# Performance work log

Measured on AMD Instinct MI355X. Metric: run time of the kernel, lower is better.

Reference implementation:

```python
import jax, jax.numpy as jnp
import numpy as np

NUM_LATENTS = 8192
LATENT_DIM = 256


def setup_inputs() -> dict:
    key = jax.random.key(0)
    kx, kw = jax.random.split(key)
    x = jax.random.normal(kx, (32, 512, LATENT_DIM), dtype=jnp.float32)
    # codebook init: uniform(-1/K, 1/K), matching nn.Embedding init in the module
    bound = 1.0 / NUM_LATENTS
    codebook = jax.random.uniform(
        kw, (NUM_LATENTS, LATENT_DIM), dtype=jnp.float32, minval=-bound, maxval=bound
    )
    return {"x": x, "codebook": codebook}


def reference(x, codebook):
    # torch.cdist(x, W) followed by argmin. Since sqrt is monotone, argmin over
    # squared Euclidean distance gives identical indices; we expand
    x2 = jnp.sum(x * x, axis=-1, keepdims=True)              # [B, T, 1]
    w2 = jnp.sum(codebook * codebook, axis=-1)               # [K]
    xw = jnp.einsum("btd,kd->btk", x, codebook)              # [B, T, K]
    dist2 = x2 - 2.0 * xw + w2                               # [B, T, K]
    indices = jnp.argmin(dist2, axis=-1)                     # [B, T] int
    z = codebook[indices]                                    # [B, T, D]
    # straight-through estimator: z_q = x + stop_grad(z - x)
    z_q = x + jax.lax.stop_gradient(z - x)
    return (z_q, z, x, indices)
```

## Files before the change

### kernel.cpp

```cpp
#include <hip/hip_runtime.h>
#include <hip/hip_bf16.h>
#include <cstddef>
#include <cstdint>

#define M_TOK   16384
#define N_CODE  8192
#define K_DIM   256
#define NSPLIT  4
#define BM      128
#define BN      128
#define BK      32

typedef short bf16x8 __attribute__((ext_vector_type(8)));
typedef float f32x4  __attribute__((ext_vector_type(4)));

__device__ __forceinline__ unsigned short f2bf_rne(float f) {
    unsigned u = __float_as_uint(f);
    unsigned r = u + 0x7FFFu + ((u >> 16) & 1u);
    return (unsigned short)(r >> 16);
}
__device__ __forceinline__ float bf2f(unsigned short h) {
    union { unsigned u; float f; } c; c.u = ((unsigned)h) << 16; return c.f;
}

__device__ __forceinline__ void gload16(const void* g, void* l) {
    __builtin_amdgcn_global_load_lds(
        (const __attribute__((address_space(1))) void*)g,
        (__attribute__((address_space(3))) void*)l, 16, 0, 0);
}

__global__ void vq_prep(const float* __restrict__ x, const float* __restrict__ cb,
                        unsigned short* __restrict__ xh, unsigned short* __restrict__ xl,
                        unsigned short* __restrict__ wh, unsigned short* __restrict__ wl,
                        float* __restrict__ x2, float* __restrict__ w2) {
    int gt   = blockIdx.x * blockDim.x + threadIdx.x;
    int row  = gt >> 6;
    int lane = gt & 63;
    if (row >= M_TOK + N_CODE) return;
    const float* src; unsigned short *dh, *dl; float* dn;
    if (row < M_TOK) {
        src = x + (size_t)row * K_DIM;
        dh = xh + (size_t)row * K_DIM; dl = xl + (size_t)row * K_DIM; dn = x2 + row;
    } else {
        int r = row - M_TOK;
        src = cb + (size_t)r * K_DIM;
        dh = wh + (size_t)r * K_DIM; dl = wl + (size_t)r * K_DIM; dn = w2 + r;
    }
    float4 v = ((const float4*)src)[lane];
    unsigned short h0 = f2bf_rne(v.x), h1 = f2bf_rne(v.y);
    unsigned short h2 = f2bf_rne(v.z), h3 = f2bf_rne(v.w);
    unsigned short l0 = f2bf_rne(v.x - bf2f(h0)), l1 = f2bf_rne(v.y - bf2f(h1));
    unsigned short l2 = f2bf_rne(v.z - bf2f(h2)), l3 = f2bf_rne(v.w - bf2f(h3));
    ushort4 hv; hv.x = h0; hv.y = h1; hv.z = h2; hv.w = h3;
    ushort4 lv; lv.x = l0; lv.y = l1; lv.z = l2; lv.w = l3;
    ((ushort4*)dh)[lane] = hv;
    ((ushort4*)dl)[lane] = lv;
    float s = v.x*v.x + v.y*v.y + v.z*v.z + v.w*v.w;
    #pragma unroll
    for (int off = 32; off > 0; off >>= 1) s += __shfl_down(s, off);
    if (lane == 0) *dn = s;
}

__global__ __launch_bounds__(256, 2)
void vq_main_mfma(const unsigned short* __restrict__ xh, const unsigned short* __restrict__ xl,
                  const unsigned short* __restrict__ wh, const unsigned short* __restrict__ wl,
                  const float* __restrict__ x2, const float* __restrict__ w2,
                  float* __restrict__ pminv, int* __restrict__ pmini) {
    __shared__ unsigned short xh_s[BM][BK];
    __shared__ unsigned short xl_s[BM][BK];
    __shared__ unsigned short wh_s[BN][BK];
    __shared__ unsigned short wl_s[BN][BK];
    __shared__ float red_d[BM][2];
    __shared__ int   red_i[BM][2];

    const int split = blockIdx.x;
    const int mtile = blockIdx.y;
    const int gm    = mtile * BM;
    const int tid   = threadIdx.x;
    const int w     = tid >> 6;
    const int lane  = tid & 63;
    const int wr    = w >> 1;
    const int wc    = w & 1;
    const int quad  = lane >> 4;
    const int l15   = lane & 15;

    const int w32   = w * 32;
    const int srow  = (lane >> 2);
    const int sc16  = (lane & 3) * 16;

    float x2r[16];
    #pragma unroll
    for (int rt = 0; rt < 4; ++rt)
        #pragma unroll
        for (int reg = 0; reg < 4; ++reg)
            x2r[rt*4+reg] = x2[gm + wr*64 + rt*16 + quad*4 + reg];

    float minv[16];
    int   mini[16];
    #pragma unroll
    for (int i = 0; i < 16; ++i) { minv[i] = 3.4e38f; mini[i] = 0; }

    const char* xhp = (const char*)xh;
    const char* xlp = (const char*)xl;
    const char* whp = (const char*)wh;
    const char* wlp = (const char*)wl;

    const int tiles = (N_CODE / NSPLIT) / BN;
    for (int tile = 0; tile < tiles; ++tile) {
        const int nb = split * (N_CODE / NSPLIT) + tile * BN;

        f32x4 acc[4][4];
        #pragma unroll
        for (int rt = 0; rt < 4; ++rt)
            #pragma unroll
            for (int ct = 0; ct < 4; ++ct)
                acc[rt][ct] = (f32x4){0.f, 0.f, 0.f, 0.f};

        for (int kc = 0; kc < K_DIM / BK; ++kc) {
            __syncthreads();
            #pragma unroll
            for (int i = 0; i < 2; ++i) {
                int r = w32 + i * 16 + srow;
                size_t xoff = (size_t)(gm + r) * (K_DIM*2) + kc*(BK*2) + sc16;
                size_t woff = (size_t)(nb + r) * (K_DIM*2) + kc*(BK*2) + sc16;
                unsigned ldso = (unsigned)(w32 + i * 16) * (BK*2);
                gload16(xhp + xoff, (char*)&xh_s[0][0] + ldso);
                gload16(xlp + xoff, (char*)&xl_s[0][0] + ldso);
                gload16(whp + woff, (char*)&wh_s[0][0] + ldso);
                gload16(wlp + woff, (char*)&wl_s[0][0] + ldso);
            }
            __syncthreads();

            bf16x8 ah[4], al[4], bh[4], bl[4];
            const int ko = quad * 16;
            #pragma unroll
            for (int rt = 0; rt < 4; ++rt) {
                int off = (wr*64 + rt*16 + l15) * (BK*2) + ko;
                ah[rt] = *(const bf16x8*)((const char*)&xh_s[0][0] + off);
                al[rt] = *(const bf16x8*)((const char*)&xl_s[0][0] + off);
            }
            #pragma unroll
            for (int ct = 0; ct < 4; ++ct) {
                int off = (wc*64 + ct*16 + l15) * (BK*2) + ko;
                bh[ct] = *(const bf16x8*)((const char*)&wh_s[0][0] + off);
                bl[ct] = *(const bf16x8*)((const char*)&wl_s[0][0] + off);
            }
            #pragma unroll
            for (int rt = 0; rt < 4; ++rt)
                #pragma unroll
                for (int ct = 0; ct < 4; ++ct) {
                    acc[rt][ct] = __builtin_amdgcn_mfma_f32_16x16x32_bf16(al[rt], bh[ct], acc[rt][ct], 0, 0, 0);
                    acc[rt][ct] = __builtin_amdgcn_mfma_f32_16x16x32_bf16(ah[rt], bl[ct], acc[rt][ct], 0, 0, 0);
                    acc[rt][ct] = __builtin_amdgcn_mfma_f32_16x16x32_bf16(ah[rt], bh[ct], acc[rt][ct], 0, 0, 0);
                }
        }

        float w2c[4];
        int   cidx[4];
        #pragma unroll
        for (int ct = 0; ct < 4; ++ct) {
            cidx[ct] = nb + wc*64 + ct*16 + l15;
            w2c[ct]  = w2[cidx[ct]];
        }
        #pragma unroll
        for (int rt = 0; rt < 4; ++rt)
            #pragma unroll
            for (int ct = 0; ct < 4; ++ct) {
                #pragma unroll
                for (int reg = 0; reg < 4; ++reg) {
                    float d = (x2r[rt*4+reg] - 2.0f * acc[rt][ct][reg]) + w2c[ct];
                    int r16 = rt*4 + reg;
                    if (d < minv[r16]) { minv[r16] = d; mini[r16] = cidx[ct]; }
                }
            }
    }

    #pragma unroll
    for (int r16 = 0; r16 < 16; ++r16) {
        float d  = minv[r16];
        int   ix = mini[r16];
        #pragma unroll
        for (int off = 1; off < 16; off <<= 1) {
            float od = __shfl_xor(d, off);
            int   oi = __shfl_xor(ix, off);
            if (od < d || (od == d && oi < ix)) { d = od; ix = oi; }
        }
        if (l15 == 0) {
            int row_local = wr*64 + (r16 >> 2)*16 + quad*4 + (r16 & 3);
            red_d[row_local][wc] = d;
            red_i[row_local][wc] = ix;
        }
    }
    __syncthreads();
    if (tid < BM) {
        float d0 = red_d[tid][0], d1 = red_d[tid][1];
        int   i0 = red_i[tid][0], i1 = red_i[tid][1];
        float d; int ix;
        if (d1 < d0 || (d1 == d0 && i1 < i0)) { d = d1; ix = i1; } else { d = d0; ix = i0; }
        pminv[(size_t)(gm + tid) * NSPLIT + split] = d;
        pmini[(size_t)(gm + tid) * NSPLIT + split] = ix;
    }
}

__global__ void vq_reduce(const float* __restrict__ pminv, const int* __restrict__ pmini,
                          int* __restrict__ idxf) {
    int m = blockIdx.x * blockDim.x + threadIdx.x;
    if (m >= M_TOK) return;
    float best = pminv[(size_t)m * NSPLIT];
    int   bi   = pmini[(size_t)m * NSPLIT];
    #pragma unroll
    for (int s = 1; s < NSPLIT; ++s) {
        float d  = pminv[(size_t)m * NSPLIT + s];
        int   i2 = pmini[(size_t)m * NSPLIT + s];
        if (d < best || (d == best && i2 < bi)) { best = d; bi = i2; }
    }
    idxf[m] = bi;
}

__global__ void vq_gather(const float* __restrict__ x, const float* __restrict__ cb,
                          const int* __restrict__ idxf, float* __restrict__ out) {
    int t = blockIdx.x * blockDim.x + threadIdx.x;
    int m = t >> 6;
    int q = t & 63;
    int idx = idxf[m];
    float4 xv = ((const float4*)x)[t];
    float4 zv = ((const float4*)cb)[(size_t)idx * 64 + q];
    float4 zq;
    zq.x = xv.x + (zv.x - xv.x);
    zq.y = xv.y + (zv.y - xv.y);
    zq.z = xv.z + (zv.z - xv.z);
    zq.w = xv.w + (zv.w - xv.w);
    float4* o = (float4*)out;
    const int ELEM4 = M_TOK * 64;
    o[t]           = zq;
    o[t + ELEM4]   = zv;
    o[t + 2*ELEM4] = xv;
    if (q == 0) out[(size_t)3 * M_TOK * K_DIM + m] = (float)idx;
}

extern "C" void kernel_launch(void* const* d_in, const int* in_sizes, int n_in,
                              void* d_out, int out_size, void* d_ws, size_t ws_size,
                              hipStream_t stream) {
    const float* x  = (const float*)d_in[0];
    const float* cb = (const float*)d_in[1];
    float* out = (float*)d_out;

    char* p = (char*)d_ws;
    unsigned short* xh = (unsigned short*)p;  p += (size_t)M_TOK  * K_DIM * 2;
    unsigned short* xl = (unsigned short*)p;  p += (size_t)M_TOK  * K_DIM * 2;
    unsigned short* wh = (unsigned short*)p;  p += (size_t)N_CODE * K_DIM * 2;
    unsigned short* wl = (unsigned short*)p;  p += (size_t)N_CODE * K_DIM * 2;
    float* x2    = (float*)p;  p += (size_t)M_TOK * 4;
    float* w2    = (float*)p;  p += (size_t)N_CODE * 4;
    float* pminv = (float*)p;  p += (size_t)M_TOK * NSPLIT * 4;
    int*   pmini = (int*)p;    p += (size_t)M_TOK * NSPLIT * 4;
    int*   idxf  = (int*)p;

    {
        int waves = M_TOK + N_CODE;
        vq_prep<<<(waves * 64 + 255) / 256, 256, 0, stream>>>(x, cb, xh, xl, wh, wl, x2, w2);
    }
    {
        dim3 grid(NSPLIT, M_TOK / BM);
        vq_main_mfma<<<grid, 256, 0, stream>>>(xh, xl, wh, wl, x2, w2, pminv, pmini);
    }
    vq_reduce<<<(M_TOK + 255) / 256, 256, 0, stream>>>(pminv, pmini, idxf);
    {
        int t = M_TOK * (K_DIM / 4);
        vq_gather<<<t / 256, 256, 0, stream>>>(x, cb, idxf, out);
    }
}
```

Baseline: 304.8 us.

## Double codebook splits, raise occupancy, fold split reduction into gather

Raises the number of codebook splits from 4 to 8, which doubles the main GEMM grid. It also raises launch bounds to 4 blocks per SM so more blocks can be resident at once. The separate reduce kernel is removed: the gather kernel now reads the 8 partial minima and reduces them with a wave shuffle butterfly, which saves one launch and one pass through global memory. In exchange, the higher occupancy bound may force register spills in the MFMA kernel, and each tile of x is reloaded across twice as many splits.

```diff
diff --git a/kernel.cpp b/kernel.cpp
--- a/kernel.cpp
+++ b/kernel.cpp
@@ -6,7 +6,7 @@
 #define M_TOK   16384
 #define N_CODE  8192
 #define K_DIM   256
-#define NSPLIT  4
+#define NSPLIT  8
 #define BM      128
 #define BN      128
 #define BK      32
@@ -61,7 +61,7 @@
     if (lane == 0) *dn = s;
 }
 
-__global__ __launch_bounds__(256, 2)
+__global__ __launch_bounds__(256, 4)
 void vq_main_mfma(const unsigned short* __restrict__ xh, const unsigned short* __restrict__ xl,
                   const unsigned short* __restrict__ wh, const unsigned short* __restrict__ wl,
                   const float* __restrict__ x2, const float* __restrict__ w2,
@@ -202,29 +202,24 @@
     }
 }
 
-__global__ void vq_reduce(const float* __restrict__ pminv, const int* __restrict__ pmini,
-                          int* __restrict__ idxf) {
-    int m = blockIdx.x * blockDim.x + threadIdx.x;
-    if (m >= M_TOK) return;
-    float best = pminv[(size_t)m * NSPLIT];
-    int   bi   = pmini[(size_t)m * NSPLIT];
-    #pragma unroll
-    for (int s = 1; s < NSPLIT; ++s) {
-        float d  = pminv[(size_t)m * NSPLIT + s];
-        int   i2 = pmini[(size_t)m * NSPLIT + s];
-        if (d < best || (d == best && i2 < bi)) { best = d; bi = i2; }
-    }
-    idxf[m] = bi;
-}
-
 __global__ void vq_gather(const float* __restrict__ x, const float* __restrict__ cb,
-                          const int* __restrict__ idxf, float* __restrict__ out) {
+                          const float* __restrict__ pminv, const int* __restrict__ pmini,
+                          float* __restrict__ out) {
     int t = blockIdx.x * blockDim.x + threadIdx.x;
     int m = t >> 6;
     int q = t & 63;
-    int idx = idxf[m];
+
+    float d  = pminv[(size_t)m * NSPLIT + (q & 7)];
+    int   ix = pmini[(size_t)m * NSPLIT + (q & 7)];
+    #pragma unroll
+    for (int off = 1; off < NSPLIT; off <<= 1) {
+        float od = __shfl_xor(d, off);
+        int   oi = __shfl_xor(ix, off);
+        if (od < d || (od == d && oi < ix)) { d = od; ix = oi; }
+    }
+
     float4 xv = ((const float4*)x)[t];
-    float4 zv = ((const float4*)cb)[(size_t)idx * 64 + q];
+    float4 zv = ((const float4*)cb)[(size_t)ix * 64 + q];
     float4 zq;
     zq.x = xv.x + (zv.x - xv.x);
     zq.y = xv.y + (zv.y - xv.y);
@@ -235,7 +230,7 @@
     o[t]           = zq;
     o[t + ELEM4]   = zv;
     o[t + 2*ELEM4] = xv;
-    if (q == 0) out[(size_t)3 * M_TOK * K_DIM + m] = (float)idx;
+    if (q == 0) out[(size_t)3 * M_TOK * K_DIM + m] = (float)ix;
 }
 
 extern "C" void kernel_launch(void* const* d_in, const int* in_sizes, int n_in,
@@ -254,7 +249,6 @@
     float* w2    = (float*)p;  p += (size_t)N_CODE * 4;
     float* pminv = (float*)p;  p += (size_t)M_TOK * NSPLIT * 4;
     int*   pmini = (int*)p;    p += (size_t)M_TOK * NSPLIT * 4;
-    int*   idxf  = (int*)p;
 
     {
         int waves = M_TOK + N_CODE;
@@ -264,9 +258,8 @@
         dim3 grid(NSPLIT, M_TOK / BM);
         vq_main_mfma<<<grid, 256, 0, stream>>>(xh, xl, wh, wl, x2, w2, pminv, pmini);
     }
-    vq_reduce<<<(M_TOK + 255) / 256, 256, 0, stream>>>(pminv, pmini, idxf);
     {
         int t = M_TOK * (K_DIM / 4);
-        vq_gather<<<t / 256, 256, 0, stream>>>(x, cb, idxf, out);
-    }
-}
+        vq_gather<<<t / 256, 256, 0, stream>>>(x, cb, pminv, pmini, out);
+    }
+}
```

New measurement: 504.3 us. 65.4% more time.
